# Kernel optimization log

Measured on AMD Instinct MI355X. Metric: run time of the kernel, lower is better.

The kernel has to match this reference:

```python
import jax, jax.numpy as jnp
import numpy as np

N, C = 8192, 4096
EPS = 1e-12


def setup_inputs() -> dict:
    key = jax.random.key(0)
    kx, ky = jax.random.split(key)
    act_X = jax.random.normal(kx, (N, C), dtype=jnp.float32)
    act_Y = jax.random.normal(ky, (N, C), dtype=jnp.float32)
    return {"act_X": act_X, "act_Y": act_Y}


def reference(act_X, act_Y):
    # softmax over class dim (dim=1 in the torch module)
    probs_X = jax.nn.softmax(act_X, axis=1)  # [N, C]
    probs_Y = jax.nn.softmax(act_Y, axis=1)  # [N, C]

    # approximate_entropy_cu: mean per-sample Shannon entropy (nats)
    entropy = jnp.mean(-jnp.sum(probs_X * jnp.log(probs_X + EPS), axis=1))

    # approximate_mi_cu: plug-in MI from batch-averaged joint distribution
    n = probs_X.shape[0]
    joint = jnp.einsum('nc,nd->cd', probs_X, probs_Y) / n  # [C, C]
    marg_X = jnp.mean(probs_X, axis=0)  # [C]
    marg_Y = jnp.mean(probs_Y, axis=0)  # [C]
    log_ratio = jnp.log(joint + EPS) - (jnp.log(marg_X + EPS)[:, None]
                                        + jnp.log(marg_Y + EPS)[None, :])
    mi = jnp.sum(joint * log_ratio)

    return jnp.stack([entropy, mi])  # shape [2]
```

## Files before the change

### kernel.cpp

```cpp
#include <hip/hip_runtime.h>
#include <hip/hip_bf16.h>
#include <stdint.h>

#define NROWS 8192
#define CDIM  4096
#define KDIM  8192
#define EPS   1e-12f

typedef __attribute__((ext_vector_type(8)))  int   v8i;
typedef __attribute__((ext_vector_type(4)))  int   v4i;
typedef __attribute__((ext_vector_type(4)))  float f32x4;
typedef __attribute__((ext_vector_type(2)))  float f32x2;

__device__ inline float wave_sum(float v) {
#pragma unroll
    for (int o = 32; o > 0; o >>= 1) v += __shfl_xor(v, o, 64);
    return v;
}
__device__ inline float wave_max(float v) {
#pragma unroll
    for (int o = 32; o > 0; o >>= 1) v = fmaxf(v, __shfl_xor(v, o, 64));
    return v;
}

__global__ __launch_bounds__(256) void row_quant_kernel(const float* __restrict__ X,
                                                        const float* __restrict__ Y,
                                                        unsigned char* __restrict__ QX,
                                                        unsigned char* __restrict__ QY,
                                                        float* __restrict__ entPart) {
    const int t = threadIdx.x, lane = t & 63, wave = t >> 6;
    const int row = blockIdx.x * 4 + wave;
    const bool isY = blockIdx.y != 0;
    const float4* s4 = (const float4*)((isY ? Y : X) + (size_t)row * CDIM);
    unsigned int* dst = (unsigned int*)((isY ? QY : QX) + (size_t)row * CDIM);
    float4 v[16];
#pragma unroll
    for (int i = 0; i < 16; i++) v[i] = s4[i * 64 + lane];
    float m = -3.0e38f;
#pragma unroll
    for (int i = 0; i < 16; i++)
        m = fmaxf(m, fmaxf(fmaxf(v[i].x, v[i].y), fmaxf(v[i].z, v[i].w)));
    m = wave_max(m);
    float Z = 0.f, S = 0.f;
#pragma unroll
    for (int i = 0; i < 16; i++) {
        float e;
        e = __expf(v[i].x - m); Z += e; S += e * v[i].x; v[i].x = e;
        e = __expf(v[i].y - m); Z += e; S += e * v[i].y; v[i].y = e;
        e = __expf(v[i].z - m); Z += e; S += e * v[i].z; v[i].z = e;
        e = __expf(v[i].w - m); Z += e; S += e * v[i].w; v[i].w = e;
    }
    Z = wave_sum(Z); S = wave_sum(S);
    __shared__ float sent[4];
    if (lane == 0) sent[wave] = m + __logf(Z) - S / Z;
    const float sc = 512.0f / Z;
#pragma unroll
    for (int i = 0; i < 16; i++) {
        unsigned int w0 = (unsigned int)__builtin_amdgcn_cvt_pk_fp8_f32(
            v[i].x * sc, v[i].y * sc, 0, false);
        w0 = (unsigned int)__builtin_amdgcn_cvt_pk_fp8_f32(
            v[i].z * sc, v[i].w * sc, (int)w0, true);
        dst[i * 64 + lane] = w0;
    }
    __syncthreads();
    if (t == 0 && !isY)
        entPart[blockIdx.x] = sent[0] + sent[1] + sent[2] + sent[3];
}

__global__ __launch_bounds__(256) void transpose_marg_kernel(
        const unsigned char* __restrict__ QX, const unsigned char* __restrict__ QY,
        unsigned char* __restrict__ QXT, unsigned char* __restrict__ QYT,
        float* __restrict__ margX, float* __restrict__ margY) {
    const bool isY = blockIdx.z != 0;
    const unsigned char* __restrict__ Q = isY ? QY : QX;
    unsigned char* __restrict__ QT = isY ? QYT : QXT;
    float* __restrict__ marg = isY ? margY : margX;

    __shared__ __align__(16) unsigned char tile[128 * 128];
    __shared__ float smarg[128];
    const int t = threadIdx.x;
    const int c0 = blockIdx.x * 128, n0 = blockIdx.y * 128;
    if (t < 128) smarg[t] = 0.f;
    __syncthreads();
    const int cq = (t & 31) * 4;
    const int nq = (t >> 5) * 16;
    const unsigned char* src = Q + (size_t)(n0 + nq) * CDIM + c0 + cq;
    unsigned int u[16];
#pragma unroll
    for (int i = 0; i < 16; i++)
        u[i] = *(const unsigned int*)(src + (size_t)i * CDIM);
#pragma unroll
    for (int j = 0; j < 4; j++) {
        const unsigned int sel = (unsigned)j | ((unsigned)(j + 4) << 8);
        unsigned int d0, d1, d2, d3;
        {
            unsigned int p01 = __builtin_amdgcn_perm(u[1], u[0], sel);
            unsigned int p23 = __builtin_amdgcn_perm(u[3], u[2], sel);
            d0 = __builtin_amdgcn_perm(p23, p01, 0x05040100u);
        }
        {
            unsigned int p01 = __builtin_amdgcn_perm(u[5], u[4], sel);
            unsigned int p23 = __builtin_amdgcn_perm(u[7], u[6], sel);
            d1 = __builtin_amdgcn_perm(p23, p01, 0x05040100u);
        }
        {
            unsigned int p01 = __builtin_amdgcn_perm(u[9], u[8], sel);
            unsigned int p23 = __builtin_amdgcn_perm(u[11], u[10], sel);
            d2 = __builtin_amdgcn_perm(p23, p01, 0x05040100u);
        }
        {
            unsigned int p01 = __builtin_amdgcn_perm(u[13], u[12], sel);
            unsigned int p23 = __builtin_amdgcn_perm(u[15], u[14], sel);
            d3 = __builtin_amdgcn_perm(p23, p01, 0x05040100u);
        }
        const int r = cq + j;
        uint4 o; o.x = d0; o.y = d1; o.z = d2; o.w = d3;
        *(uint4*)&tile[r * 128 + ((((nq >> 4) ^ ((r >> 2) & 7))) << 4)] = o;
        float s = 0.f;
        f32x2 a;
        a = __builtin_amdgcn_cvt_pk_f32_fp8((int)d0, false); s += a.x + a.y;
        a = __builtin_amdgcn_cvt_pk_f32_fp8((int)d0, true);  s += a.x + a.y;
        a = __builtin_amdgcn_cvt_pk_f32_fp8((int)d1, false); s += a.x + a.y;
        a = __builtin_amdgcn_cvt_pk_f32_fp8((int)d1, true);  s += a.x + a.y;
        a = __builtin_amdgcn_cvt_pk_f32_fp8((int)d2, false); s += a.x + a.y;
        a = __builtin_amdgcn_cvt_pk_f32_fp8((int)d2, true);  s += a.x + a.y;
        a = __builtin_amdgcn_cvt_pk_f32_fp8((int)d3, false); s += a.x + a.y;
        a = __builtin_amdgcn_cvt_pk_f32_fp8((int)d3, true);  s += a.x + a.y;
        atomicAdd(&smarg[r], s);
    }
    __syncthreads();
#pragma unroll
    for (int p = 0; p < 4; p++) {
        const int r = p * 32 + (t >> 3);
        const int k = t & 7;
        uint4 o = *(const uint4*)&tile[r * 128 + (((k ^ ((r >> 2) & 7))) << 4)];
        *(uint4*)(QT + (size_t)(c0 + r) * KDIM + n0 + k * 16) = o;
    }
    if (t < 128) atomicAdd(&marg[c0 + t], smarg[t]);
}

#define GLD16(g, l)                                                                   \
    __builtin_amdgcn_global_load_lds((const __attribute__((address_space(1))) unsigned int*)(g), \
                                     (__attribute__((address_space(3))) unsigned int*)(l), 16, 0, 0)

#define BUFSZ 65536
#define BOFS  32768

__global__ __launch_bounds__(512, 2) void gemm_mi_kernel(const unsigned char* __restrict__ A,
                                                         const unsigned char* __restrict__ B,
                                                         float* __restrict__ S_out) {
    __shared__ __align__(16) unsigned char lds[131072];
    const int t = threadIdx.x;
    const int lane = t & 63, wave = t >> 6;
    const int m0 = blockIdx.x * 256, n0 = blockIdx.y * 256;

    const int srow = wave * 32 + (lane >> 3);
    const int gcol = ((lane & 7) ^ (lane >> 3)) * 16;
    const unsigned char* ga = A + (size_t)(m0 + srow) * KDIM + gcol;
    const unsigned char* gb = B + (size_t)(n0 + srow) * KDIM + gcol;
    const int loff = wave * 4096 + lane * 16;

    const int wm = (wave >> 2) * 128, wn = (wave & 3) * 64;
    const int fr = lane & 15, quad = lane >> 4, sw = fr & 7;
    const int off0 = ((2 * quad)     ^ sw) * 16;
    const int off1 = ((2 * quad + 1) ^ sw) * 16;

    f32x4 acc[8][4];
#pragma unroll
    for (int i = 0; i < 8; i++)
#pragma unroll
        for (int j = 0; j < 4; j++) { acc[i][j][0] = 0.f; acc[i][j][1] = 0.f; acc[i][j][2] = 0.f; acc[i][j][3] = 0.f; }

#pragma unroll
    for (int i = 0; i < 4; i++) {
        GLD16(ga + (size_t)i * 8 * KDIM, lds + loff + i * 1024);
        GLD16(gb + (size_t)i * 8 * KDIM, lds + BOFS + loff + i * 1024);
    }

    int cur = 0;
    for (int tt = 0; tt < KDIM / 128; ++tt) {
        if (tt + 1 < KDIM / 128) {
            const int nb = (cur ^ 1) * BUFSZ;
            const int kn = (tt + 1) * 128;
#pragma unroll
            for (int i = 0; i < 4; i++) {
                GLD16(ga + (size_t)i * 8 * KDIM + kn, lds + nb + loff + i * 1024);
                GLD16(gb + (size_t)i * 8 * KDIM + kn, lds + nb + BOFS + loff + i * 1024);
            }
            asm volatile("s_waitcnt vmcnt(8)" ::: "memory");
        } else {
            asm volatile("s_waitcnt vmcnt(0)" ::: "memory");
        }
        asm volatile("s_barrier" ::: "memory");
        __builtin_amdgcn_sched_barrier(0);

        const unsigned char* base = lds + cur * BUFSZ;
        v8i bg[4];
#pragma unroll
        for (int j = 0; j < 4; j++) {
            const unsigned char* pB = base + BOFS + (wn + j * 16 + fr) * 128;
            v4i lo = *(const v4i*)(pB + off0);
            v4i hi = *(const v4i*)(pB + off1);
            bg[j][0] = lo[0]; bg[j][1] = lo[1]; bg[j][2] = lo[2]; bg[j][3] = lo[3];
            bg[j][4] = hi[0]; bg[j][5] = hi[1]; bg[j][6] = hi[2]; bg[j][7] = hi[3];
        }
        __builtin_amdgcn_s_setprio(1);
#pragma unroll
        for (int i = 0; i < 8; i++) {
            const unsigned char* pA = base + (wm + i * 16 + fr) * 128;
            v4i lo = *(const v4i*)(pA + off0);
            v4i hi = *(const v4i*)(pA + off1);
            v8i af;
            af[0] = lo[0]; af[1] = lo[1]; af[2] = lo[2]; af[3] = lo[3];
            af[4] = hi[0]; af[5] = hi[1]; af[6] = hi[2]; af[7] = hi[3];
#pragma unroll
            for (int j = 0; j < 4; j++)
                acc[i][j] = __builtin_amdgcn_mfma_scale_f32_16x16x128_f8f6f4(
                    af, bg[j], acc[i][j], 0 , 0 ,
                    0, 0x7f , 0, 0x7f );
        }
        __builtin_amdgcn_s_setprio(0);
        __builtin_amdgcn_sched_barrier(0);
        asm volatile("s_waitcnt lgkmcnt(0)" ::: "memory");
        asm volatile("s_barrier" ::: "memory");
        __builtin_amdgcn_sched_barrier(0);
        cur ^= 1;
    }

    const float invS = 4.656612873077393e-10f;
    float loc = 0.f;
#pragma unroll
    for (int i = 0; i < 8; i++)
#pragma unroll
        for (int j = 0; j < 4; j++)
#pragma unroll
            for (int r = 0; r < 4; r++) {
                float v = acc[i][j][r] * invS;
                loc += v * __logf(v + EPS);
            }
    loc = wave_sum(loc);
    __shared__ float sred[8];
    if (lane == 0) sred[wave] = loc;
    __syncthreads();
    if (t == 0) {
        float s = 0.f;
#pragma unroll
        for (int w = 0; w < 8; w++) s += sred[w];
        atomicAdd(S_out, s);
    }
}

__global__ __launch_bounds__(256) void finalize_kernel(const float* __restrict__ accums,
                                                       const float* __restrict__ entPart,
                                                       const float* __restrict__ margX,
                                                       const float* __restrict__ margY,
                                                       float* __restrict__ out) {
    const int t = threadIdx.x;
    const int lane = t & 63, w = t >> 6;
    const float invN = 1.0f / 8192.0f;
    const float invM = 1.0f / 4194304.0f;
    float sx = 0.f, sy = 0.f, se = 0.f;
    for (int c = t; c < CDIM; c += 256) {
        float mx = margX[c] * invM;
        float my = margY[c] * invM;
        sx += mx * __logf(mx + EPS);
        sy += my * __logf(my + EPS);
    }
    for (int c = t; c < 2048; c += 256) se += entPart[c];
    sx = wave_sum(sx); sy = wave_sum(sy); se = wave_sum(se);
    __shared__ float rx[4], ry[4], re[4];
    if (lane == 0) { rx[w] = sx; ry[w] = sy; re[w] = se; }
    __syncthreads();
    if (t == 0) {
        float SX = rx[0] + rx[1] + rx[2] + rx[3];
        float SY = ry[0] + ry[1] + ry[2] + ry[3];
        float SE = re[0] + re[1] + re[2] + re[3];
        out[0] = SE * invN;
        out[1] = accums[0] - SX - SY;
    }
}

extern "C" void kernel_launch(void* const* d_in, const int* in_sizes, int n_in,
                              void* d_out, int out_size, void* d_ws, size_t ws_size,
                              hipStream_t stream) {
    const float* X = (const float*)d_in[0];
    const float* Y = (const float*)d_in[1];
    char* ws = (char*)d_ws;
    unsigned char* QX  = (unsigned char*)ws;
    unsigned char* QY  = (unsigned char*)(ws + 33554432ll);
    unsigned char* QXT = (unsigned char*)(ws + 67108864ll);
    unsigned char* QYT = (unsigned char*)(ws + 100663296ll);
    float* margX = (float*)(ws + 134217728ll);
    float* margY = (float*)(ws + 134234112ll);
    float* accums = (float*)(ws + 134250496ll);
    float* entPart = (float*)(ws + 134250752ll);

    hipMemsetAsync(ws + 134217728ll, 0, 2 * 16384 + 256, stream);

    row_quant_kernel<<<dim3(2048, 2), 256, 0, stream>>>(X, Y, QX, QY, entPart);
    transpose_marg_kernel<<<dim3(CDIM / 128, NROWS / 128, 2), 256, 0, stream>>>(
        QX, QY, QXT, QYT, margX, margY);
    gemm_mi_kernel<<<dim3(CDIM / 256, CDIM / 256), 512, 0, stream>>>(QXT, QYT, &accums[0]);
    finalize_kernel<<<1, 256, 0, stream>>>(accums, entPart, margX, margY, (float*)d_out);
}
```

Measured before the change: 457.3 us.

## Split FP8 GEMM k-step into four phases interleaving prefetch loads with MFMA

The main GEMM loop used to issue all eight global-to-LDS prefetch loads for the next k-tile at the top of each iteration, then run all 32 MFMAs. It now issues one pair of prefetch loads per phase and splits the MFMA work into four phases of two A-fragments each, with barriers and lgkmcnt waits between phases. The aim is to spread global memory traffic across the compute and keep the LDS reads for each phase close to their MFMAs. The cost is several extra workgroup barriers per k-step, which can stall waves and cut MFMA issue density.

```diff
diff --git a/kernel.cpp b/kernel.cpp
--- a/kernel.cpp
+++ b/kernel.cpp
@@ -146,6 +146,30 @@
 #define BUFSZ 65536
 #define BOFS  32768
 
+__device__ __forceinline__ v8i pack8(const unsigned char* p, int off0, int off1) {
+    v4i lo = *(const v4i*)(p + off0);
+    v4i hi = *(const v4i*)(p + off1);
+    v8i a;
+    a[0] = lo[0]; a[1] = lo[1]; a[2] = lo[2]; a[3] = lo[3];
+    a[4] = hi[0]; a[5] = hi[1]; a[6] = hi[2]; a[7] = hi[3];
+    return a;
+}
+
+template <int P>
+__device__ __forceinline__ void phase_mfma(const v8i& a0, const v8i& a1,
+                                           const v8i (&bg)[4], f32x4 (&acc)[8][4]) {
+    __builtin_amdgcn_s_setprio(1);
+#pragma unroll
+    for (int j = 0; j < 4; j++)
+        acc[2 * P][j] = __builtin_amdgcn_mfma_scale_f32_16x16x128_f8f6f4(
+            a0, bg[j], acc[2 * P][j], 0, 0, 0, 0x7f, 0, 0x7f);
+#pragma unroll
+    for (int j = 0; j < 4; j++)
+        acc[2 * P + 1][j] = __builtin_amdgcn_mfma_scale_f32_16x16x128_f8f6f4(
+            a1, bg[j], acc[2 * P + 1][j], 0, 0, 0, 0x7f, 0, 0x7f);
+    __builtin_amdgcn_s_setprio(0);
+}
+
 __global__ __launch_bounds__(512, 2) void gemm_mi_kernel(const unsigned char* __restrict__ A,
                                                          const unsigned char* __restrict__ B,
                                                          float* __restrict__ S_out) {
@@ -179,48 +203,77 @@
 
     int cur = 0;
     for (int tt = 0; tt < KDIM / 128; ++tt) {
-        if (tt + 1 < KDIM / 128) {
-            const int nb = (cur ^ 1) * BUFSZ;
-            const int kn = (tt + 1) * 128;
-#pragma unroll
-            for (int i = 0; i < 4; i++) {
-                GLD16(ga + (size_t)i * 8 * KDIM + kn, lds + nb + loff + i * 1024);
-                GLD16(gb + (size_t)i * 8 * KDIM + kn, lds + nb + BOFS + loff + i * 1024);
-            }
-            asm volatile("s_waitcnt vmcnt(8)" ::: "memory");
+        const unsigned char* base = lds + cur * BUFSZ;
+        unsigned char* nbuf = lds + (cur ^ 1) * BUFSZ;
+        const size_t kn = (size_t)(tt + 1) * 128;
+        const bool more = (tt + 1 < KDIM / 128);
+
+        if (more) {
+            GLD16(ga + kn, nbuf + loff);
+            GLD16(gb + kn, nbuf + BOFS + loff);
+            asm volatile("s_waitcnt vmcnt(2)" ::: "memory");
         } else {
             asm volatile("s_waitcnt vmcnt(0)" ::: "memory");
         }
         asm volatile("s_barrier" ::: "memory");
         __builtin_amdgcn_sched_barrier(0);
-
-        const unsigned char* base = lds + cur * BUFSZ;
         v8i bg[4];
 #pragma unroll
-        for (int j = 0; j < 4; j++) {
-            const unsigned char* pB = base + BOFS + (wn + j * 16 + fr) * 128;
-            v4i lo = *(const v4i*)(pB + off0);
-            v4i hi = *(const v4i*)(pB + off1);
-            bg[j][0] = lo[0]; bg[j][1] = lo[1]; bg[j][2] = lo[2]; bg[j][3] = lo[3];
-            bg[j][4] = hi[0]; bg[j][5] = hi[1]; bg[j][6] = hi[2]; bg[j][7] = hi[3];
-        }
-        __builtin_amdgcn_s_setprio(1);
-#pragma unroll
-        for (int i = 0; i < 8; i++) {
-            const unsigned char* pA = base + (wm + i * 16 + fr) * 128;
-            v4i lo = *(const v4i*)(pA + off0);
-            v4i hi = *(const v4i*)(pA + off1);
-            v8i af;
-            af[0] = lo[0]; af[1] = lo[1]; af[2] = lo[2]; af[3] = lo[3];
-            af[4] = hi[0]; af[5] = hi[1]; af[6] = hi[2]; af[7] = hi[3];
-#pragma unroll
-            for (int j = 0; j < 4; j++)
-                acc[i][j] = __builtin_amdgcn_mfma_scale_f32_16x16x128_f8f6f4(
-                    af, bg[j], acc[i][j], 0 , 0 ,
-                    0, 0x7f , 0, 0x7f );
-        }
-        __builtin_amdgcn_s_setprio(0);
-        __builtin_amdgcn_sched_barrier(0);
+        for (int j = 0; j < 4; j++)
+            bg[j] = pack8(base + BOFS + (wn + j * 16 + fr) * 128, off0, off1);
+        {
+            v8i a0 = pack8(base + (wm + 0 * 16 + fr) * 128, off0, off1);
+            v8i a1 = pack8(base + (wm + 1 * 16 + fr) * 128, off0, off1);
+            asm volatile("s_barrier" ::: "memory");
+            asm volatile("s_waitcnt lgkmcnt(0)" ::: "memory");
+            __builtin_amdgcn_sched_barrier(0);
+            phase_mfma<0>(a0, a1, bg, acc);
+        }
+        asm volatile("s_barrier" ::: "memory");
+        __builtin_amdgcn_sched_barrier(0);
+
+        if (more) {
+            GLD16(ga + (size_t)8 * KDIM + kn, nbuf + loff + 1024);
+            GLD16(gb + (size_t)8 * KDIM + kn, nbuf + BOFS + loff + 1024);
+        }
+        {
+            v8i a0 = pack8(base + (wm + 2 * 16 + fr) * 128, off0, off1);
+            v8i a1 = pack8(base + (wm + 3 * 16 + fr) * 128, off0, off1);
+            asm volatile("s_barrier" ::: "memory");
+            asm volatile("s_waitcnt lgkmcnt(0)" ::: "memory");
+            __builtin_amdgcn_sched_barrier(0);
+            phase_mfma<1>(a0, a1, bg, acc);
+        }
+        asm volatile("s_barrier" ::: "memory");
+        __builtin_amdgcn_sched_barrier(0);
+
+        if (more) {
+            GLD16(ga + (size_t)16 * KDIM + kn, nbuf + loff + 2048);
+            GLD16(gb + (size_t)16 * KDIM + kn, nbuf + BOFS + loff + 2048);
+        }
+        {
+            v8i a0 = pack8(base + (wm + 4 * 16 + fr) * 128, off0, off1);
+            v8i a1 = pack8(base + (wm + 5 * 16 + fr) * 128, off0, off1);
+            asm volatile("s_barrier" ::: "memory");
+            asm volatile("s_waitcnt lgkmcnt(0)" ::: "memory");
+            __builtin_amdgcn_sched_barrier(0);
+            phase_mfma<2>(a0, a1, bg, acc);
+        }
+        asm volatile("s_barrier" ::: "memory");
+        __builtin_amdgcn_sched_barrier(0);
+
+        if (more) {
+            GLD16(ga + (size_t)24 * KDIM + kn, nbuf + loff + 3072);
+            GLD16(gb + (size_t)24 * KDIM + kn, nbuf + BOFS + loff + 3072);
+        }
+        {
+            v8i a0 = pack8(base + (wm + 6 * 16 + fr) * 128, off0, off1);
+            v8i a1 = pack8(base + (wm + 7 * 16 + fr) * 128, off0, off1);
+            asm volatile("s_barrier" ::: "memory");
+            asm volatile("s_waitcnt lgkmcnt(0)" ::: "memory");
+            __builtin_amdgcn_sched_barrier(0);
+            phase_mfma<3>(a0, a1, bg, acc);
+        }
         asm volatile("s_waitcnt lgkmcnt(0)" ::: "memory");
         asm volatile("s_barrier" ::: "memory");
         __builtin_amdgcn_sched_barrier(0);
```

Result: slower. 520.4 us (+13.8%).
